# Kernel tuning notes

Hardware: AMD Instinct MI355X
Metric: run time of the kernel (lower is better)

Reference implementation:

```python
import jax, jax.numpy as jnp
import numpy as np

LN_EPS = 1e-5  # torch.nn.LayerNorm default


def setup_inputs() -> dict:
    key = jax.random.key(0)
    k1, k2, k3 = jax.random.split(key, 3)
    B, N, F, D = 8, 2048, 128, 128
    A_hat = jax.random.uniform(k1, (B, N, N), dtype=jnp.float32)
    X = jax.random.normal(k2, (B, N, F), dtype=jnp.float32)
    W = jax.random.normal(k3, (D, F), dtype=jnp.float32) * (1.0 / np.sqrt(F))
    b = jnp.zeros((D,), dtype=jnp.float32)
    gamma = jnp.ones((D,), dtype=jnp.float32)
    beta = jnp.zeros((D,), dtype=jnp.float32)
    return {"A_hat": A_hat, "X": X, "W": W, "b": b, "gamma": gamma, "beta": beta}


def reference(A_hat, X, W, b, gamma, beta):
    # batched aggregation: H[b] = A_hat[b] @ X[b]   (torch loop over batch, vectorized here)
    H = jnp.einsum('bnm,bmf->bnf', A_hat, X)
    # linear: torch nn.Linear stores W as [out, in]
    H = jnp.einsum('bnf,df->bnd', H, W) + b
    # LayerNorm over last dim, then ReLU (dropout p=0 -> identity)
    mu = jnp.mean(H, axis=-1, keepdims=True)
    var = jnp.mean((H - mu) ** 2, axis=-1, keepdims=True)
    Hn = (H - mu) * jax.lax.rsqrt(var + LN_EPS) * gamma + beta
    return jax.nn.relu(Hn)
```

## Files before the change

### kernel.cpp

```cpp
#include <hip/hip_runtime.h>
#include <stdint.h>

#define B_DIM 8
#define N_DIM 2048
#define F_DIM 128
#define LN_EPS 1e-5f

typedef __attribute__((ext_vector_type(8))) short short8;
typedef __attribute__((ext_vector_type(4))) float floatx4;

__device__ __forceinline__ ushort f2bf(float f) {
    union { float f; uint32_t u; } c;
    c.f = f;
    uint32_t u = c.u;
    return (ushort)((u + 0x7FFFu + ((u >> 16) & 1u)) >> 16);
}

__device__ __forceinline__ uint32_t pk2bf(float a, float b) {
    union { float f; uint32_t u; } x, y;
    x.f = a; y.f = b;
    return ((x.u + 0x8000u) >> 16) | ((y.u + 0x8000u) & 0xFFFF0000u);
}

__device__ __forceinline__ short8 pack8(float4 lo, float4 hi) {
    union { uint32_t u[4]; short8 s; } r;
    r.u[0] = pk2bf(lo.x, lo.y);
    r.u[1] = pk2bf(lo.z, lo.w);
    r.u[2] = pk2bf(hi.x, hi.y);
    r.u[3] = pk2bf(hi.z, hi.w);
    return r.s;
}

__device__ __forceinline__ void load_lds16(const ushort* g, ushort* l) {
    __builtin_amdgcn_global_load_lds(
        (const __attribute__((address_space(1))) void*)g,
        (__attribute__((address_space(3))) void*)l,
        16, 0, 0);
}

__global__ __launch_bounds__(256) void k_transpose(const float* __restrict__ X,
                                                   ushort* __restrict__ Xt) {
    __shared__ ushort tile[64 * 65];
    const int t = threadIdx.x;
    const int b = blockIdx.z;
    const int k0 = blockIdx.x * 64;
    const int f0 = blockIdx.y * 64;

#pragma unroll
    for (int p = 0; p < 2; ++p) {
        int idx = p * 256 + t;
        int kk = idx >> 3;
        int ff = (idx & 7) * 8;
        const float* src = X + (((size_t)b * N_DIM) + k0 + kk) * F_DIM + f0 + ff;
        float4 v0 = *(const float4*)(src);
        float4 v1 = *(const float4*)(src + 4);
        ushort* d = tile + kk * 65 + ff;
        d[0] = f2bf(v0.x); d[1] = f2bf(v0.y); d[2] = f2bf(v0.z); d[3] = f2bf(v0.w);
        d[4] = f2bf(v1.x); d[5] = f2bf(v1.y); d[6] = f2bf(v1.z); d[7] = f2bf(v1.w);
    }
    __syncthreads();

    union U { uint4 v; ushort s[8]; };
#pragma unroll
    for (int p = 0; p < 2; ++p) {
        int idx = p * 256 + t;
        int f2 = idx >> 3;
        int kk2 = (idx & 7) * 8;
        U u;
#pragma unroll
        for (int j = 0; j < 8; ++j) u.s[j] = tile[(kk2 + j) * 65 + f2];
        *(uint4*)(Xt + (((size_t)b * F_DIM) + f0 + f2) * N_DIM + k0 + kk2) = u.v;
    }
}

__global__ __launch_bounds__(256) void k_fused(const float* __restrict__ A,
                                               const ushort* __restrict__ Xt,
                                               const float* __restrict__ W,
                                               const float* __restrict__ bias,
                                               const float* __restrict__ gamma,
                                               const float* __restrict__ beta,
                                               float* __restrict__ out) {
    __shared__ __align__(16) ushort As[32 * 128];
    __shared__ __align__(16) ushort Bs[128 * 128];
    __shared__ __align__(16) ushort Ht[32 * 136];
    __shared__ float Pt[32][132];

    const int t = threadIdx.x;
    const int lane = t & 63;
    const int w = t >> 6;
    const int q = lane >> 4;
    const int mr = lane & 15;

    const int bid = blockIdx.x;
    const int bb = bid & 7;
    const int m0 = (bid >> 3) * 32;

    const float* Ab = A + ((size_t)bb * N_DIM + m0) * N_DIM;
    const ushort* Xb = Xt + (size_t)bb * F_DIM * N_DIM;

    const int arow = t >> 3;
    const int asw_ = arow & 7;
    const float* a_src = Ab + (size_t)arow * N_DIM + (t & 7) * 16;
    ushort* a_dst0 = As + arow * 128 + ((((t & 7) * 2) ^ asw_) * 8);
    ushort* a_dst1 = As + arow * 128 + ((((t & 7) * 2 + 1) ^ asw_) * 8);

    const ushort* b_src[8];
    ushort* b_dst[8];
#pragma unroll
    for (int p = 0; p < 8; ++p) {
        int c = p * 256 + t;
        int n = c >> 4;
        int kc = (c & 15) ^ (n & 7);
        b_src[p] = Xb + (size_t)n * N_DIM + kc * 8;
        b_dst[p] = Bs + c * 8;
    }

    floatx4 acc[2][2];
#pragma unroll
    for (int i = 0; i < 2; ++i)
#pragma unroll
        for (int j = 0; j < 2; ++j) acc[i][j] = (floatx4){0.f, 0.f, 0.f, 0.f};

    for (int k0 = 0; k0 < N_DIM; k0 += 128) {
        float4 v0 = ((const float4*)(a_src + k0))[0];
        float4 v1 = ((const float4*)(a_src + k0))[1];
        float4 v2 = ((const float4*)(a_src + k0))[2];
        float4 v3 = ((const float4*)(a_src + k0))[3];
#pragma unroll
        for (int p = 0; p < 8; ++p) load_lds16(b_src[p] + k0, b_dst[p]);
        *(short8*)a_dst0 = pack8(v0, v1);
        *(short8*)a_dst1 = pack8(v2, v3);
        __syncthreads();

#pragma unroll
        for (int ks = 0; ks < 4; ++ks) {
            short8 af[2], bf[2];
#pragma unroll
            for (int i = 0; i < 2; ++i) {
                int m = mr + i * 16;
                af[i] = *(const short8*)(As + m * 128 + (((ks * 4 + q) ^ (m & 7)) * 8));
            }
#pragma unroll
            for (int j = 0; j < 2; ++j) {
                int n = w * 32 + j * 16 + mr;
                bf[j] = *(const short8*)(Bs + n * 128 + (((ks * 4 + q) ^ (n & 7)) * 8));
            }
#pragma unroll
            for (int i = 0; i < 2; ++i)
#pragma unroll
                for (int j = 0; j < 2; ++j)
                    acc[i][j] = __builtin_amdgcn_mfma_f32_16x16x32_bf16(
                        af[i], bf[j], acc[i][j], 0, 0, 0);
        }
        __syncthreads();
    }

#pragma unroll
    for (int j = 0; j < 2; ++j) {
        int col = w * 32 + j * 16 + mr;
#pragma unroll
        for (int r = 0; r < 4; ++r) {
            Ht[(q * 4 + r) * 136 + col] = f2bf(acc[0][j][r]);
            Ht[(16 + q * 4 + r) * 136 + col] = f2bf(acc[1][j][r]);
        }
    }
    __syncthreads();

    floatx4 p[2][2];
#pragma unroll
    for (int i = 0; i < 2; ++i)
#pragma unroll
        for (int j = 0; j < 2; ++j) p[i][j] = (floatx4){0.f, 0.f, 0.f, 0.f};

#pragma unroll
    for (int ks = 0; ks < 4; ++ks) {
        short8 ha0 = *(const short8*)(Ht + mr * 136 + ks * 32 + q * 8);
        short8 ha1 = *(const short8*)(Ht + (mr + 16) * 136 + ks * 32 + q * 8);
#pragma unroll
        for (int j = 0; j < 2; ++j) {
            const float* wp = W + (w * 32 + j * 16 + mr) * F_DIM + ks * 32 + q * 8;
            short8 wb = pack8(((const float4*)wp)[0], ((const float4*)wp)[1]);
            p[0][j] = __builtin_amdgcn_mfma_f32_16x16x32_bf16(ha0, wb, p[0][j], 0, 0, 0);
            p[1][j] = __builtin_amdgcn_mfma_f32_16x16x32_bf16(ha1, wb, p[1][j], 0, 0, 0);
        }
    }

#pragma unroll
    for (int j = 0; j < 2; ++j) {
        int col = w * 32 + j * 16 + mr;
        float bcol = bias[col];
#pragma unroll
        for (int r = 0; r < 4; ++r) {
            Pt[q * 4 + r][col] = p[0][j][r] + bcol;
            Pt[16 + q * 4 + r][col] = p[1][j][r] + bcol;
        }
    }
    __syncthreads();

    const int row = t >> 3;
    const int seg = t & 7;
    float v[16];
    float s = 0.f, s2 = 0.f;
#pragma unroll
    for (int u = 0; u < 16; ++u) {
        v[u] = Pt[row][seg * 16 + u];
        s += v[u];
        s2 += v[u] * v[u];
    }
    s += __shfl_xor(s, 1);  s2 += __shfl_xor(s2, 1);
    s += __shfl_xor(s, 2);  s2 += __shfl_xor(s2, 2);
    s += __shfl_xor(s, 4);  s2 += __shfl_xor(s2, 4);
    float mu = s * (1.0f / 128.0f);
    float var = s2 * (1.0f / 128.0f) - mu * mu;
    float rs = rsqrtf(var + LN_EPS);

    float4 o[4];
    float* of = (float*)o;
#pragma unroll
    for (int u = 0; u < 16; ++u) {
        int d = seg * 16 + u;
        float y = (v[u] - mu) * rs * gamma[d] + beta[d];
        of[u] = fmaxf(y, 0.0f);
    }
    float4* dst = (float4*)(out + ((size_t)bb * N_DIM + m0 + row) * F_DIM + seg * 16);
    dst[0] = o[0]; dst[1] = o[1]; dst[2] = o[2]; dst[3] = o[3];
}

extern "C" void kernel_launch(void* const* d_in, const int* in_sizes, int n_in,
                              void* d_out, int out_size, void* d_ws, size_t ws_size,
                              hipStream_t stream) {
    const float* A     = (const float*)d_in[0];
    const float* X     = (const float*)d_in[1];
    const float* W     = (const float*)d_in[2];
    const float* bias  = (const float*)d_in[3];
    const float* gamma = (const float*)d_in[4];
    const float* beta  = (const float*)d_in[5];
    float* out = (float*)d_out;

    ushort* Xt = (ushort*)d_ws;

    k_transpose<<<dim3(32, 2, 8), 256, 0, stream>>>(X, Xt);
    k_fused<<<dim3(512), 256, 0, stream>>>(A, Xt, W, bias, gamma, beta, out);
}
```

Before: 213.2 us.

## Split aggregation GEMM along K and move linear+LayerNorm to separate kernel

Splits the A@X reduction into two halves so twice as many blocks run, writing fp32 partial results to workspace. A new kernel sums the partials, stages W as bf16 in shared memory, and does the linear, LayerNorm and ReLU. Adds register prefetch of the next A tile in the main loop. This raises occupancy and latency hiding at the cost of extra partial-sum global traffic and a kernel launch.

```diff
diff --git a/kernel.cpp b/kernel.cpp
--- a/kernel.cpp
+++ b/kernel.cpp
@@ -5,6 +5,8 @@
 #define N_DIM 2048
 #define F_DIM 128
 #define LN_EPS 1e-5f
+#define NROWS (B_DIM * N_DIM)
+#define HP_STRIDE ((size_t)NROWS * F_DIM)
 
 typedef __attribute__((ext_vector_type(8))) short short8;
 typedef __attribute__((ext_vector_type(4))) float floatx4;
@@ -73,17 +75,11 @@
     }
 }
 
-__global__ __launch_bounds__(256) void k_fused(const float* __restrict__ A,
-                                               const ushort* __restrict__ Xt,
-                                               const float* __restrict__ W,
-                                               const float* __restrict__ bias,
-                                               const float* __restrict__ gamma,
-                                               const float* __restrict__ beta,
-                                               float* __restrict__ out) {
+__global__ __launch_bounds__(256) void k_gemm_splitk(const float* __restrict__ A,
+                                                     const ushort* __restrict__ Xt,
+                                                     float* __restrict__ Hp) {
     __shared__ __align__(16) ushort As[32 * 128];
     __shared__ __align__(16) ushort Bs[128 * 128];
-    __shared__ __align__(16) ushort Ht[32 * 136];
-    __shared__ float Pt[32][132];
 
     const int t = threadIdx.x;
     const int lane = t & 63;
@@ -93,16 +89,18 @@
 
     const int bid = blockIdx.x;
     const int bb = bid & 7;
-    const int m0 = (bid >> 3) * 32;
+    const int idx = bid >> 3;
+    const int kh = idx & 1;
+    const int m0 = (idx >> 1) * 32;
+    const int kst = kh * 1024;
 
     const float* Ab = A + ((size_t)bb * N_DIM + m0) * N_DIM;
     const ushort* Xb = Xt + (size_t)bb * F_DIM * N_DIM;
 
     const int arow = t >> 3;
-    const int asw_ = arow & 7;
-    const float* a_src = Ab + (size_t)arow * N_DIM + (t & 7) * 16;
-    ushort* a_dst0 = As + arow * 128 + ((((t & 7) * 2) ^ asw_) * 8);
-    ushort* a_dst1 = As + arow * 128 + ((((t & 7) * 2 + 1) ^ asw_) * 8);
+    const float* a_src = Ab + (size_t)arow * N_DIM + (t & 7) * 16 + kst;
+    ushort* a_dst0 = As + arow * 128 + ((((t & 7) * 2) ^ (arow & 7)) * 8);
+    ushort* a_dst1 = As + arow * 128 + ((((t & 7) * 2 + 1) ^ (arow & 7)) * 8);
 
     const ushort* b_src[8];
     ushort* b_dst[8];
@@ -111,7 +109,7 @@
         int c = p * 256 + t;
         int n = c >> 4;
         int kc = (c & 15) ^ (n & 7);
-        b_src[p] = Xb + (size_t)n * N_DIM + kc * 8;
+        b_src[p] = Xb + (size_t)n * N_DIM + kc * 8 + kst;
         b_dst[p] = Bs + c * 8;
     }
 
@@ -121,15 +119,22 @@
 #pragma unroll
         for (int j = 0; j < 2; ++j) acc[i][j] = (floatx4){0.f, 0.f, 0.f, 0.f};
 
-    for (int k0 = 0; k0 < N_DIM; k0 += 128) {
-        float4 v0 = ((const float4*)(a_src + k0))[0];
-        float4 v1 = ((const float4*)(a_src + k0))[1];
-        float4 v2 = ((const float4*)(a_src + k0))[2];
-        float4 v3 = ((const float4*)(a_src + k0))[3];
+    float4 c0 = ((const float4*)a_src)[0];
+    float4 c1 = ((const float4*)a_src)[1];
+    float4 c2 = ((const float4*)a_src)[2];
+    float4 c3 = ((const float4*)a_src)[3];
+
+    for (int it = 0; it < 8; ++it) {
+        const int k0 = it * 128;
+        const float* pa = a_src + (it < 7 ? k0 + 128 : k0);
+        float4 n0 = ((const float4*)pa)[0];
+        float4 n1 = ((const float4*)pa)[1];
+        float4 n2 = ((const float4*)pa)[2];
+        float4 n3 = ((const float4*)pa)[3];
 #pragma unroll
         for (int p = 0; p < 8; ++p) load_lds16(b_src[p] + k0, b_dst[p]);
-        *(short8*)a_dst0 = pack8(v0, v1);
-        *(short8*)a_dst1 = pack8(v2, v3);
+        *(short8*)a_dst0 = pack8(c0, c1);
+        *(short8*)a_dst1 = pack8(c2, c3);
         __syncthreads();
 
 #pragma unroll
@@ -153,16 +158,61 @@
                         af[i], bf[j], acc[i][j], 0, 0, 0);
         }
         __syncthreads();
-    }
-
-#pragma unroll
-    for (int j = 0; j < 2; ++j) {
-        int col = w * 32 + j * 16 + mr;
-#pragma unroll
-        for (int r = 0; r < 4; ++r) {
-            Ht[(q * 4 + r) * 136 + col] = f2bf(acc[0][j][r]);
-            Ht[(16 + q * 4 + r) * 136 + col] = f2bf(acc[1][j][r]);
-        }
+        c0 = n0; c1 = n1; c2 = n2; c3 = n3;
+    }
+
+    float* Hb = Hp + (size_t)kh * HP_STRIDE + ((size_t)bb * N_DIM + m0) * F_DIM;
+#pragma unroll
+    for (int i = 0; i < 2; ++i)
+#pragma unroll
+        for (int j = 0; j < 2; ++j) {
+            int col = w * 32 + j * 16 + mr;
+#pragma unroll
+            for (int r = 0; r < 4; ++r)
+                Hb[(size_t)(i * 16 + q * 4 + r) * F_DIM + col] = acc[i][j][r];
+        }
+}
+
+__global__ __launch_bounds__(256) void k_linear_ln(const float* __restrict__ Hp,
+                                                   const float* __restrict__ W,
+                                                   const float* __restrict__ bias,
+                                                   const float* __restrict__ gamma,
+                                                   const float* __restrict__ beta,
+                                                   float* __restrict__ out) {
+    __shared__ __align__(16) ushort Ws[128 * 136];
+    __shared__ __align__(16) ushort Hs[32 * 136];
+    __shared__ __align__(16) float Pt[32][132];
+
+    const int t = threadIdx.x;
+    const int lane = t & 63;
+    const int w = t >> 6;
+    const int q = lane >> 4;
+    const int mr = lane & 15;
+    const size_t r0 = (size_t)blockIdx.x * 32;
+
+#pragma unroll
+    for (int p = 0; p < 8; ++p) {
+        int c = p * 256 + t;
+        int d = c >> 4;
+        int ff = (c & 15) * 8;
+        const float* src = W + d * 128 + ff;
+        *(short8*)(Ws + d * 136 + ff) =
+            pack8(((const float4*)src)[0], ((const float4*)src)[1]);
+    }
+#pragma unroll
+    for (int p = 0; p < 2; ++p) {
+        int c = p * 256 + t;
+        int m = c >> 4;
+        int ff = (c & 15) * 8;
+        const float* h0 = Hp + (r0 + m) * F_DIM + ff;
+        const float* h1 = h0 + HP_STRIDE;
+        float4 a0 = ((const float4*)h0)[0];
+        float4 a1 = ((const float4*)h0)[1];
+        float4 b0 = ((const float4*)h1)[0];
+        float4 b1 = ((const float4*)h1)[1];
+        float4 s0 = {a0.x + b0.x, a0.y + b0.y, a0.z + b0.z, a0.w + b0.w};
+        float4 s1 = {a1.x + b1.x, a1.y + b1.y, a1.z + b1.z, a1.w + b1.w};
+        *(short8*)(Hs + m * 136 + ff) = pack8(s0, s1);
     }
     __syncthreads();
 
@@ -174,12 +224,11 @@
 
 #pragma unroll
     for (int ks = 0; ks < 4; ++ks) {
-        short8 ha0 = *(const short8*)(Ht + mr * 136 + ks * 32 + q * 8);
-        short8 ha1 = *(const short8*)(Ht + (mr + 16) * 136 + ks * 32 + q * 8);
+        short8 ha0 = *(const short8*)(Hs + mr * 136 + ks * 32 + q * 8);
+        short8 ha1 = *(const short8*)(Hs + (mr + 16) * 136 + ks * 32 + q * 8);
 #pragma unroll
         for (int j = 0; j < 2; ++j) {
-            const float* wp = W + (w * 32 + j * 16 + mr) * F_DIM + ks * 32 + q * 8;
-            short8 wb = pack8(((const float4*)wp)[0], ((const float4*)wp)[1]);
+            short8 wb = *(const short8*)(Ws + (w * 32 + j * 16 + mr) * 136 + ks * 32 + q * 8);
             p[0][j] = __builtin_amdgcn_mfma_f32_16x16x32_bf16(ha0, wb, p[0][j], 0, 0, 0);
             p[1][j] = __builtin_amdgcn_mfma_f32_16x16x32_bf16(ha1, wb, p[1][j], 0, 0, 0);
         }
@@ -222,7 +271,7 @@
         float y = (v[u] - mu) * rs * gamma[d] + beta[d];
         of[u] = fmaxf(y, 0.0f);
     }
-    float4* dst = (float4*)(out + ((size_t)bb * N_DIM + m0 + row) * F_DIM + seg * 16);
+    float4* dst = (float4*)(out + (r0 + row) * F_DIM + seg * 16);
     dst[0] = o[0]; dst[1] = o[1]; dst[2] = o[2]; dst[3] = o[3];
 }
 
@@ -238,7 +287,9 @@
     float* out = (float*)d_out;
 
     ushort* Xt = (ushort*)d_ws;
+    float* Hp = (float*)((char*)d_ws + (size_t)B_DIM * F_DIM * N_DIM * 2);
 
     k_transpose<<<dim3(32, 2, 8), 256, 0, stream>>>(X, Xt);
-    k_fused<<<dim3(512), 256, 0, stream>>>(A, Xt, W, bias, gamma, beta, out);
-}
+    k_gemm_splitk<<<dim3(1024), 256, 0, stream>>>(A, Xt, Hp);
+    k_linear_ln<<<dim3(512), 256, 0, stream>>>(Hp, W, bias, gamma, beta, out);
+}
```

Result: slower. 218.9 us (+2.7%).

## Double M tile to 64 rows with 512 threads, prefetch A and alias LDS

Applied to the files above, without the earlier changes.

Each block now covers 64 output rows with 8 waves in a 2x4 arrangement, so every Xt tile staged in LDS is reused across twice as many A rows. This halves the redundant reads of Xt. The next A chunk is loaded into registers one iteration ahead to hide global latency, and the epilogue buffers now share LDS with the mainloop buffers through a union. The cost is half as many blocks (256 on a large-CU GPU), which lowers parallelism, plus more register pressure from the prefetch.

```diff
diff --git a/kernel.cpp b/kernel.cpp
--- a/kernel.cpp
+++ b/kernel.cpp
@@ -73,42 +73,47 @@
     }
 }
 
-__global__ __launch_bounds__(256) void k_fused(const float* __restrict__ A,
-                                               const ushort* __restrict__ Xt,
-                                               const float* __restrict__ W,
-                                               const float* __restrict__ bias,
-                                               const float* __restrict__ gamma,
-                                               const float* __restrict__ beta,
-                                               float* __restrict__ out) {
-    __shared__ __align__(16) ushort As[32 * 128];
-    __shared__ __align__(16) ushort Bs[128 * 128];
-    __shared__ __align__(16) ushort Ht[32 * 136];
-    __shared__ float Pt[32][132];
+union SMem {
+    struct { ushort As[64 * 128]; ushort Bs[128 * 128]; } k;
+    struct { ushort Ht[64 * 136]; float Pt[64][132]; } e;
+};
+
+__global__ __launch_bounds__(512, 2) void k_fused(const float* __restrict__ A,
+                                                  const ushort* __restrict__ Xt,
+                                                  const float* __restrict__ W,
+                                                  const float* __restrict__ bias,
+                                                  const float* __restrict__ gamma,
+                                                  const float* __restrict__ beta,
+                                                  float* __restrict__ out) {
+    __shared__ __align__(16) SMem sm;
+    ushort* As = sm.k.As;
+    ushort* Bs = sm.k.Bs;
 
     const int t = threadIdx.x;
     const int lane = t & 63;
     const int w = t >> 6;
+    const int wm = w & 1;
+    const int wn = w >> 1;
     const int q = lane >> 4;
     const int mr = lane & 15;
 
     const int bid = blockIdx.x;
     const int bb = bid & 7;
-    const int m0 = (bid >> 3) * 32;
+    const int m0 = (bid >> 3) * 64;
 
     const float* Ab = A + ((size_t)bb * N_DIM + m0) * N_DIM;
     const ushort* Xb = Xt + (size_t)bb * F_DIM * N_DIM;
 
-    const int arow = t >> 3;
-    const int asw_ = arow & 7;
-    const float* a_src = Ab + (size_t)arow * N_DIM + (t & 7) * 16;
-    ushort* a_dst0 = As + arow * 128 + ((((t & 7) * 2) ^ asw_) * 8);
-    ushort* a_dst1 = As + arow * 128 + ((((t & 7) * 2 + 1) ^ asw_) * 8);
-
-    const ushort* b_src[8];
-    ushort* b_dst[8];
-#pragma unroll
-    for (int p = 0; p < 8; ++p) {
-        int c = p * 256 + t;
+    const int ar = t >> 3;
+    const float* a_src = Ab + (size_t)ar * N_DIM + (t & 7) * 16;
+    ushort* a_dst0 = As + ar * 128 + ((((t & 7) * 2) ^ (ar & 7)) * 8);
+    ushort* a_dst1 = As + ar * 128 + ((((t & 7) * 2 + 1) ^ (ar & 7)) * 8);
+
+    const ushort* b_src[4];
+    ushort* b_dst[4];
+#pragma unroll
+    for (int p = 0; p < 4; ++p) {
+        int c = p * 512 + t;
         int n = c >> 4;
         int kc = (c & 15) ^ (n & 7);
         b_src[p] = Xb + (size_t)n * N_DIM + kc * 8;
@@ -121,15 +126,22 @@
 #pragma unroll
         for (int j = 0; j < 2; ++j) acc[i][j] = (floatx4){0.f, 0.f, 0.f, 0.f};
 
-    for (int k0 = 0; k0 < N_DIM; k0 += 128) {
-        float4 v0 = ((const float4*)(a_src + k0))[0];
-        float4 v1 = ((const float4*)(a_src + k0))[1];
-        float4 v2 = ((const float4*)(a_src + k0))[2];
-        float4 v3 = ((const float4*)(a_src + k0))[3];
-#pragma unroll
-        for (int p = 0; p < 8; ++p) load_lds16(b_src[p] + k0, b_dst[p]);
-        *(short8*)a_dst0 = pack8(v0, v1);
-        *(short8*)a_dst1 = pack8(v2, v3);
+    float4 c0 = ((const float4*)a_src)[0];
+    float4 c1 = ((const float4*)a_src)[1];
+    float4 c2 = ((const float4*)a_src)[2];
+    float4 c3 = ((const float4*)a_src)[3];
+
+    for (int it = 0; it < 16; ++it) {
+        const int k0 = it * 128;
+#pragma unroll
+        for (int p = 0; p < 4; ++p) load_lds16(b_src[p] + k0, b_dst[p]);
+        const float* pa = a_src + (it < 15 ? k0 + 128 : k0);
+        float4 n0 = ((const float4*)pa)[0];
+        float4 n1 = ((const float4*)pa)[1];
+        float4 n2 = ((const float4*)pa)[2];
+        float4 n3 = ((const float4*)pa)[3];
+        *(short8*)a_dst0 = pack8(c0, c1);
+        *(short8*)a_dst1 = pack8(c2, c3);
         __syncthreads();
 
 #pragma unroll
@@ -137,12 +149,12 @@
             short8 af[2], bf[2];
 #pragma unroll
             for (int i = 0; i < 2; ++i) {
-                int m = mr + i * 16;
+                int m = wm * 32 + i * 16 + mr;
                 af[i] = *(const short8*)(As + m * 128 + (((ks * 4 + q) ^ (m & 7)) * 8));
             }
 #pragma unroll
             for (int j = 0; j < 2; ++j) {
-                int n = w * 32 + j * 16 + mr;
+                int n = wn * 32 + j * 16 + mr;
                 bf[j] = *(const short8*)(Bs + n * 128 + (((ks * 4 + q) ^ (n & 7)) * 8));
             }
 #pragma unroll
@@ -153,17 +165,20 @@
                         af[i], bf[j], acc[i][j], 0, 0, 0);
         }
         __syncthreads();
-    }
-
-#pragma unroll
-    for (int j = 0; j < 2; ++j) {
-        int col = w * 32 + j * 16 + mr;
-#pragma unroll
-        for (int r = 0; r < 4; ++r) {
-            Ht[(q * 4 + r) * 136 + col] = f2bf(acc[0][j][r]);
-            Ht[(16 + q * 4 + r) * 136 + col] = f2bf(acc[1][j][r]);
-        }
-    }
+        c0 = n0; c1 = n1; c2 = n2; c3 = n3;
+    }
+
+    ushort* Ht = sm.e.Ht;
+
+#pragma unroll
+    for (int i = 0; i < 2; ++i)
+#pragma unroll
+        for (int j = 0; j < 2; ++j) {
+            int col = wn * 32 + j * 16 + mr;
+#pragma unroll
+            for (int r = 0; r < 4; ++r)
+                Ht[(wm * 32 + i * 16 + q * 4 + r) * 136 + col] = f2bf(acc[i][j][r]);
+        }
     __syncthreads();
 
     floatx4 p[2][2];
@@ -174,11 +189,11 @@
 
 #pragma unroll
     for (int ks = 0; ks < 4; ++ks) {
-        short8 ha0 = *(const short8*)(Ht + mr * 136 + ks * 32 + q * 8);
-        short8 ha1 = *(const short8*)(Ht + (mr + 16) * 136 + ks * 32 + q * 8);
+        short8 ha0 = *(const short8*)(Ht + (wm * 32 + mr) * 136 + ks * 32 + q * 8);
+        short8 ha1 = *(const short8*)(Ht + (wm * 32 + 16 + mr) * 136 + ks * 32 + q * 8);
 #pragma unroll
         for (int j = 0; j < 2; ++j) {
-            const float* wp = W + (w * 32 + j * 16 + mr) * F_DIM + ks * 32 + q * 8;
+            const float* wp = W + (wn * 32 + j * 16 + mr) * F_DIM + ks * 32 + q * 8;
             short8 wb = pack8(((const float4*)wp)[0], ((const float4*)wp)[1]);
             p[0][j] = __builtin_amdgcn_mfma_f32_16x16x32_bf16(ha0, wb, p[0][j], 0, 0, 0);
             p[1][j] = __builtin_amdgcn_mfma_f32_16x16x32_bf16(ha1, wb, p[1][j], 0, 0, 0);
@@ -187,12 +202,12 @@
 
 #pragma unroll
     for (int j = 0; j < 2; ++j) {
-        int col = w * 32 + j * 16 + mr;
+        int col = wn * 32 + j * 16 + mr;
         float bcol = bias[col];
 #pragma unroll
         for (int r = 0; r < 4; ++r) {
-            Pt[q * 4 + r][col] = p[0][j][r] + bcol;
-            Pt[16 + q * 4 + r][col] = p[1][j][r] + bcol;
+            sm.e.Pt[wm * 32 + q * 4 + r][col] = p[0][j][r] + bcol;
+            sm.e.Pt[wm * 32 + 16 + q * 4 + r][col] = p[1][j][r] + bcol;
         }
     }
     __syncthreads();
@@ -203,7 +218,7 @@
     float s = 0.f, s2 = 0.f;
 #pragma unroll
     for (int u = 0; u < 16; ++u) {
-        v[u] = Pt[row][seg * 16 + u];
+        v[u] = sm.e.Pt[row][seg * 16 + u];
         s += v[u];
         s2 += v[u] * v[u];
     }
@@ -240,5 +255,5 @@
     ushort* Xt = (ushort*)d_ws;
 
     k_transpose<<<dim3(32, 2, 8), 256, 0, stream>>>(X, Xt);
-    k_fused<<<dim3(512), 256, 0, stream>>>(A, Xt, W, bias, gamma, beta, out);
-}
+    k_fused<<<dim3(256), 512, 0, stream>>>(A, Xt, W, bias, gamma, beta, out);
+}
```

Result: no change. 215.7 us (+1.2%).
